# Performance work log

Measured on AMD Instinct MI355X. Metric: run time of the kernel, lower is better.

Reference implementation:

```python
import jax, jax.numpy as jnp
import numpy as np

N_NODES = 40000


def setup_inputs() -> dict:
    key = jax.random.key(0)
    k_h, k_w, k_b, k_s, k_d = jax.random.split(key, 5)
    in_feats, out_feats, n_edges = 128, 128, 640000
    h = jax.random.normal(k_h, (N_NODES, in_feats), dtype=jnp.float32)
    # nn.Linear(in_feats, out_feats): weight [out, in], bias [out]
    W = jax.random.normal(k_w, (out_feats, in_feats), dtype=jnp.float32) * (1.0 / np.sqrt(in_feats))
    b = jax.random.normal(k_b, (out_feats,), dtype=jnp.float32) * 0.01
    src = jax.random.randint(k_s, (n_edges,), 0, N_NODES, dtype=jnp.int32)
    dst = jax.random.randint(k_d, (n_edges,), 0, N_NODES, dtype=jnp.int32)
    return {"h": h, "W": W, "b": b, "src": src, "dst": dst}


def reference(h, W, b, src, dst):
    # update_all(copy_u('h','m'), sum('m','h_N')):
    # gather messages from source nodes, segment-sum into destination nodes.
    msgs = h[src]                                              # [E, in_feats] irregular gather
    agg = jax.ops.segment_sum(msgs, dst, num_segments=N_NODES)  # [N, in_feats] scatter-add
    # Source module applies the linear to h (agg is computed but unused there);
    # we return agg as a second output so the SpMM is observable.
    out = h @ W.T + b                                          # [N, out_feats]
    return out, agg
```

## Files before the change

kernel.cpp:

```cpp
#include <hip/hip_runtime.h>

#define FEAT 128
#define CAP  64

typedef short bf16x8 __attribute__((ext_vector_type(8)));
typedef float f32x4  __attribute__((ext_vector_type(4)));

__device__ __forceinline__ unsigned pack_bf16x2(float x, float y) {
    unsigned ux = __float_as_uint(x);
    ux = (ux + 0x7fffu + ((ux >> 16) & 1u)) >> 16;
    unsigned uy = __float_as_uint(y);
    uy = (uy + 0x7fffu + ((uy >> 16) & 1u)) & 0xffff0000u;
    return uy | ux;
}

__device__ __forceinline__ bf16x8 pack8(float4 a, float4 b) {
    uint4 u = make_uint4(pack_bf16x2(a.x, a.y), pack_bf16x2(a.z, a.w),
                         pack_bf16x2(b.x, b.y), pack_bf16x2(b.z, b.w));
    return __builtin_bit_cast(bf16x8, u);
}

__device__ __forceinline__ f32x4 unpack2(unsigned x, unsigned y) {
    return (f32x4){__uint_as_float(x << 16), __uint_as_float(x & 0xffff0000u),
                   __uint_as_float(y << 16), __uint_as_float(y & 0xffff0000u)};
}

__global__ __launch_bounds__(256) void fused_kernel(
    const float* __restrict__ h, const float* __restrict__ W,
    const float* __restrict__ b, const int* __restrict__ src,
    const int* __restrict__ dst, float* __restrict__ out,
    uint4* __restrict__ hb4, int* __restrict__ counts, int* __restrict__ bucket,
    int nrows, int gemm_blocks, int E)
{
    const int bid = blockIdx.x;
    const int tid = threadIdx.x;

    if (bid >= gemm_blocks) {
        int e = (bid - gemm_blocks) * 256 + tid;
        if (e < E) {
            int d = dst[e];
            int pos = atomicAdd(&counts[d], 1);
            if (pos < CAP) bucket[d * CAP + pos] = src[e];
        }
        return;
    }

    const int wid  = bid * 4 + (tid >> 6);
    const int lane = tid & 63;
    const int m    = lane & 15, quad = lane >> 4;
    const int r0g  = wid * 32;
    if (r0g >= nrows) return;

    const float4* __restrict__ h4 = (const float4*)h;
    const float4* __restrict__ W4 = (const float4*)W;

    bf16x8 af[2][4];
#pragma unroll
    for (int mt = 0; mt < 2; ++mt) {
        int gr = r0g + mt * 16 + m;
#pragma unroll
        for (int ks = 0; ks < 4; ++ks) {
            float4 a0 = h4[(size_t)gr * 32 + ks * 8 + quad * 2];
            float4 a1 = h4[(size_t)gr * 32 + ks * 8 + quad * 2 + 1];
            af[mt][ks] = pack8(a0, a1);
        }
    }

#pragma unroll
    for (int mt = 0; mt < 2; ++mt) {
        int gr = r0g + mt * 16 + m;
        if (gr < nrows) {
#pragma unroll
            for (int ks = 0; ks < 4; ++ks)
                hb4[(size_t)gr * 16 + ks * 4 + quad] = __builtin_bit_cast(uint4, af[mt][ks]);
        }
    }

    f32x4 acc[2][8];
#pragma unroll
    for (int mt = 0; mt < 2; ++mt)
#pragma unroll
        for (int n = 0; n < 8; ++n) acc[mt][n] = (f32x4){0.f, 0.f, 0.f, 0.f};

#pragma unroll
    for (int n = 0; n < 8; ++n) {
        int c = n * 16 + m;
#pragma unroll
        for (int ks = 0; ks < 4; ++ks) {
            float4 b0 = W4[(size_t)c * 32 + ks * 8 + quad * 2];
            float4 b1 = W4[(size_t)c * 32 + ks * 8 + quad * 2 + 1];
            bf16x8 bf = pack8(b0, b1);
#pragma unroll
            for (int mt = 0; mt < 2; ++mt)
                acc[mt][n] = __builtin_amdgcn_mfma_f32_16x16x32_bf16(
                    af[mt][ks], bf, acc[mt][n], 0, 0, 0);
        }
    }

#pragma unroll
    for (int n = 0; n < 8; ++n) {
        float bias = b[n * 16 + m];
#pragma unroll
        for (int mt = 0; mt < 2; ++mt)
#pragma unroll
            for (int r = 0; r < 4; ++r) {
                int gr = r0g + mt * 16 + quad * 4 + r;
                if (gr < nrows) out[(size_t)gr * FEAT + n * 16 + m] = acc[mt][n][r] + bias;
            }
    }
}

__global__ __launch_bounds__(256) void gather_bucket_kernel(
    const uint4* __restrict__ hb4, const int* __restrict__ counts,
    const int* __restrict__ bucket, float* __restrict__ agg, int N)
{
    int gid  = blockIdx.x * 256 + threadIdx.x;
    int node = gid >> 6;
    int lane = gid & 63;
    if (node >= N) return;

    int deg = counts[node];
    deg = (deg > CAP) ? CAP : deg;
    int eid = (lane < deg) ? bucket[node * CAP + lane] : 0;

    const int q = lane >> 4, ql = lane & 15;

    f32x4 al0 = {0.f,0.f,0.f,0.f}, ah0 = {0.f,0.f,0.f,0.f};
    f32x4 al1 = {0.f,0.f,0.f,0.f}, ah1 = {0.f,0.f,0.f,0.f};

    int t = 0;
    for (; t + 8 <= deg; t += 8) {
        int s0 = __shfl(eid, t + q);
        int s1 = __shfl(eid, t + 4 + q);
        uint4 v0 = hb4[(size_t)s0 * 16 + ql];
        uint4 v1 = hb4[(size_t)s1 * 16 + ql];
        al0 += unpack2(v0.x, v0.y);
        ah0 += unpack2(v0.z, v0.w);
        al1 += unpack2(v1.x, v1.y);
        ah1 += unpack2(v1.z, v1.w);
    }
    {
        int i0 = t + q, i1 = t + 4 + q;
        int s0 = __shfl(eid, i0 & 63);
        int s1 = __shfl(eid, i1 & 63);
        if (i0 < deg) {
            uint4 v = hb4[(size_t)s0 * 16 + ql];
            al0 += unpack2(v.x, v.y);
            ah0 += unpack2(v.z, v.w);
        }
        if (i1 < deg) {
            uint4 v = hb4[(size_t)s1 * 16 + ql];
            al1 += unpack2(v.x, v.y);
            ah1 += unpack2(v.z, v.w);
        }
    }
    al0 += al1; ah0 += ah1;

#pragma unroll
    for (int j = 0; j < 4; ++j) {
        al0[j] += __shfl_down(al0[j], 32);
        ah0[j] += __shfl_down(ah0[j], 32);
        al0[j] += __shfl_down(al0[j], 16);
        ah0[j] += __shfl_down(ah0[j], 16);
    }

    if (q == 0) {
        ((float4*)agg)[(size_t)node * 32 + ql * 2]     = make_float4(al0[0], al0[1], al0[2], al0[3]);
        ((float4*)agg)[(size_t)node * 32 + ql * 2 + 1] = make_float4(ah0[0], ah0[1], ah0[2], ah0[3]);
    }
}

__global__ __launch_bounds__(256, 2) void gemm_f32_kernel(
    const float* __restrict__ h, const float* __restrict__ W,
    const float* __restrict__ b, float* __restrict__ out, int nrows)
{
    __shared__ float4 wsh[128 * 8];
    __shared__ float4 hsh[64 * 8];
    const int tid = threadIdx.x;
    const int tx  = tid & 31;
    const int ty  = tid >> 5;
    const int r0  = blockIdx.x * 64;
    const float4* __restrict__ W4 = (const float4*)W;
    const float4* __restrict__ h4 = (const float4*)h;
    float acc[8][4];
#pragma unroll
    for (int i = 0; i < 8; ++i)
#pragma unroll
        for (int j = 0; j < 4; ++j) acc[i][j] = 0.f;
    for (int p = 0; p < 4; ++p) {
        if (p) __syncthreads();
#pragma unroll
        for (int l = 0; l < 4; ++l) {
            int flat = l * 256 + tid;
            int c = flat >> 3, kc = flat & 7;
            wsh[c * 8 + (kc ^ ((c >> 2) & 7))] = W4[c * 32 + p * 8 + kc];
        }
#pragma unroll
        for (int l = 0; l < 2; ++l) {
            int flat = l * 256 + tid;
            int r = flat >> 3, kc = flat & 7;
            int gr = r0 + r;
            float4 v = make_float4(0.f, 0.f, 0.f, 0.f);
            if (gr < nrows) v = h4[(size_t)gr * 32 + p * 8 + kc];
            hsh[r * 8 + (kc ^ ((r >> 2) & 7))] = v;
        }
        __syncthreads();
#pragma unroll
        for (int kc = 0; kc < 8; ++kc) {
            float4 wv[4], hv[8];
#pragma unroll
            for (int j = 0; j < 4; ++j) wv[j] = wsh[(4 * tx + j) * 8 + (kc ^ (tx & 7))];
#pragma unroll
            for (int i = 0; i < 8; ++i) {
                int r = 8 * ty + i;
                hv[i] = hsh[r * 8 + (kc ^ ((r >> 2) & 7))];
            }
#pragma unroll
            for (int i = 0; i < 8; ++i)
#pragma unroll
                for (int j = 0; j < 4; ++j) {
                    acc[i][j] += hv[i].x * wv[j].x;
                    acc[i][j] += hv[i].y * wv[j].y;
                    acc[i][j] += hv[i].z * wv[j].z;
                    acc[i][j] += hv[i].w * wv[j].w;
                }
        }
    }
    const float4 bj = ((const float4*)b)[tx];
    float4* out4 = (float4*)out;
#pragma unroll
    for (int i = 0; i < 8; ++i) {
        int gr = r0 + 8 * ty + i;
        if (gr < nrows) {
            float4 o;
            o.x = acc[i][0] + bj.x; o.y = acc[i][1] + bj.y;
            o.z = acc[i][2] + bj.z; o.w = acc[i][3] + bj.w;
            out4[(size_t)gr * 32 + tx] = o;
        }
    }
}

__global__ __launch_bounds__(256) void scatter_add_kernel(
    const float* __restrict__ h, const int* __restrict__ src,
    const int* __restrict__ dst, float* __restrict__ agg, int E)
{
    int gid  = blockIdx.x * 256 + threadIdx.x;
    int e    = gid >> 6;
    int lane = gid & 63;
    if (e >= E) return;
    int s = src[e];
    int d = dst[e];
    const float2* hp = (const float2*)(h + (size_t)s * FEAT);
    float2 v = hp[lane];
    float* ap = agg + (size_t)d * FEAT + 2 * lane;
    unsafeAtomicAdd(ap,     v.x);
    unsafeAtomicAdd(ap + 1, v.y);
}

extern "C" void kernel_launch(void* const* d_in, const int* in_sizes, int n_in,
                              void* d_out, int out_size, void* d_ws, size_t ws_size,
                              hipStream_t stream) {
    const float* h   = (const float*)d_in[0];
    const float* W   = (const float*)d_in[1];
    const float* b   = (const float*)d_in[2];
    const int*   src = (const int*)d_in[3];
    const int*   dst = (const int*)d_in[4];

    const int n = in_sizes[0] / FEAT;
    const int E = in_sizes[3];

    float* out = (float*)d_out;
    float* agg = out + (size_t)n * FEAT;

    size_t hb_bytes     = (size_t)n * FEAT * 2;
    size_t bucket_bytes = (size_t)n * CAP * 4;
    size_t counts_bytes = (size_t)n * 4;
    size_t need = hb_bytes + bucket_bytes + counts_bytes;

    if (ws_size >= need) {
        uint4* hb     = (uint4*)d_ws;
        int*   bucket = (int*)((char*)d_ws + hb_bytes);
        int*   counts = (int*)((char*)d_ws + hb_bytes + bucket_bytes);

        hipMemsetAsync(counts, 0, counts_bytes, stream);

        int gemm_blocks = (n + 127) / 128;
        int fill_blocks = (E + 255) / 256;
        fused_kernel<<<dim3(gemm_blocks + fill_blocks), dim3(256), 0, stream>>>(
            h, W, b, src, dst, out, hb, counts, bucket, n, gemm_blocks, E);

        gather_bucket_kernel<<<dim3((int)(((long long)n * 64 + 255) / 256)), dim3(256), 0, stream>>>(
            hb, counts, bucket, agg, n);
    } else {
        gemm_f32_kernel<<<dim3((n + 63) / 64), dim3(256), 0, stream>>>(h, W, b, out, n);
        hipMemsetAsync(agg, 0, (size_t)n * FEAT * sizeof(float), stream);
        int nblocks = (int)(((long long)E * 64 + 255) / 256);
        scatter_add_kernel<<<dim3(nblocks), dim3(256), 0, stream>>>(h, src, dst, agg, E);
    }
}
```

Measured before the change: 147.5 us.

## Batch bucket-fill atomics, pad counters, split GEMM columns, use nontemporal stores

The bucket-fill path now handles four edges per thread, issuing all loads, then all atomics, then all stores, so more memory operations are in flight. Per-node counters are padded to a 16-int stride to spread atomic contention across cache lines. The GEMM part now splits each 32-row tile's output columns across two waves, which doubles the GEMM blocks and halves accumulator registers, at the cost of loading h twice. Output and agg writes become nontemporal stores to avoid polluting cache. The padded counters need a larger workspace and a bigger memset.

```diff
diff --git a/kernel.cpp b/kernel.cpp
--- a/kernel.cpp
+++ b/kernel.cpp
@@ -2,6 +2,7 @@
 
 #define FEAT 128
 #define CAP  64
+#define CSTRIDE 16
 
 typedef short bf16x8 __attribute__((ext_vector_type(8)));
 typedef float f32x4  __attribute__((ext_vector_type(4)));
@@ -36,19 +37,31 @@
     const int tid = threadIdx.x;
 
     if (bid >= gemm_blocks) {
-        int e = (bid - gemm_blocks) * 256 + tid;
-        if (e < E) {
-            int d = dst[e];
-            int pos = atomicAdd(&counts[d], 1);
-            if (pos < CAP) bucket[d * CAP + pos] = src[e];
+        int base = (bid - gemm_blocks) * 1024 + tid;
+        int dk[4], sk[4], pk[4];
+#pragma unroll
+        for (int k = 0; k < 4; ++k) {
+            int e = base + k * 256;
+            if (e < E) { dk[k] = dst[e]; sk[k] = src[e]; }
+        }
+#pragma unroll
+        for (int k = 0; k < 4; ++k) {
+            int e = base + k * 256;
+            if (e < E) pk[k] = atomicAdd(&counts[dk[k] * CSTRIDE], 1);
+        }
+#pragma unroll
+        for (int k = 0; k < 4; ++k) {
+            int e = base + k * 256;
+            if (e < E && pk[k] < CAP) bucket[dk[k] * CAP + pk[k]] = sk[k];
         }
         return;
     }
 
-    const int wid  = bid * 4 + (tid >> 6);
+    const int w    = tid >> 6;
     const int lane = tid & 63;
     const int m    = lane & 15, quad = lane >> 4;
-    const int r0g  = wid * 32;
+    const int r0g  = bid * 64 + (w >> 1) * 32;
+    const int ch   = w & 1;
     if (r0g >= nrows) return;
 
     const float4* __restrict__ h4 = (const float4*)h;
@@ -66,25 +79,27 @@
         }
     }
 
-#pragma unroll
-    for (int mt = 0; mt < 2; ++mt) {
-        int gr = r0g + mt * 16 + m;
-        if (gr < nrows) {
-#pragma unroll
-            for (int ks = 0; ks < 4; ++ks)
-                hb4[(size_t)gr * 16 + ks * 4 + quad] = __builtin_bit_cast(uint4, af[mt][ks]);
-        }
-    }
-
-    f32x4 acc[2][8];
+    if (ch == 0) {
+#pragma unroll
+        for (int mt = 0; mt < 2; ++mt) {
+            int gr = r0g + mt * 16 + m;
+            if (gr < nrows) {
+#pragma unroll
+                for (int ks = 0; ks < 4; ++ks)
+                    hb4[(size_t)gr * 16 + ks * 4 + quad] = __builtin_bit_cast(uint4, af[mt][ks]);
+            }
+        }
+    }
+
+    f32x4 acc[2][4];
 #pragma unroll
     for (int mt = 0; mt < 2; ++mt)
 #pragma unroll
-        for (int n = 0; n < 8; ++n) acc[mt][n] = (f32x4){0.f, 0.f, 0.f, 0.f};
-
-#pragma unroll
-    for (int n = 0; n < 8; ++n) {
-        int c = n * 16 + m;
+        for (int n = 0; n < 4; ++n) acc[mt][n] = (f32x4){0.f, 0.f, 0.f, 0.f};
+
+#pragma unroll
+    for (int n = 0; n < 4; ++n) {
+        int c = (ch * 4 + n) * 16 + m;
 #pragma unroll
         for (int ks = 0; ks < 4; ++ks) {
             float4 b0 = W4[(size_t)c * 32 + ks * 8 + quad * 2];
@@ -98,14 +113,17 @@
     }
 
 #pragma unroll
-    for (int n = 0; n < 8; ++n) {
-        float bias = b[n * 16 + m];
+    for (int n = 0; n < 4; ++n) {
+        int col = (ch * 4 + n) * 16 + m;
+        float bias = b[col];
 #pragma unroll
         for (int mt = 0; mt < 2; ++mt)
 #pragma unroll
             for (int r = 0; r < 4; ++r) {
                 int gr = r0g + mt * 16 + quad * 4 + r;
-                if (gr < nrows) out[(size_t)gr * FEAT + n * 16 + m] = acc[mt][n][r] + bias;
+                if (gr < nrows)
+                    __builtin_nontemporal_store(acc[mt][n][r] + bias,
+                                                &out[(size_t)gr * FEAT + col]);
             }
     }
 }
@@ -119,7 +137,7 @@
     int lane = gid & 63;
     if (node >= N) return;
 
-    int deg = counts[node];
+    int deg = counts[node * CSTRIDE];
     deg = (deg > CAP) ? CAP : deg;
     int eid = (lane < deg) ? bucket[node * CAP + lane] : 0;
 
@@ -165,8 +183,9 @@
     }
 
     if (q == 0) {
-        ((float4*)agg)[(size_t)node * 32 + ql * 2]     = make_float4(al0[0], al0[1], al0[2], al0[3]);
-        ((float4*)agg)[(size_t)node * 32 + ql * 2 + 1] = make_float4(ah0[0], ah0[1], ah0[2], ah0[3]);
+        f32x4* aggv = (f32x4*)agg;
+        __builtin_nontemporal_store(al0, &aggv[(size_t)node * 32 + ql * 2]);
+        __builtin_nontemporal_store(ah0, &aggv[(size_t)node * 32 + ql * 2 + 1]);
     }
 }
 
@@ -274,7 +293,7 @@
 
     size_t hb_bytes     = (size_t)n * FEAT * 2;
     size_t bucket_bytes = (size_t)n * CAP * 4;
-    size_t counts_bytes = (size_t)n * 4;
+    size_t counts_bytes = (size_t)n * CSTRIDE * 4;
     size_t need = hb_bytes + bucket_bytes + counts_bytes;
 
     if (ws_size >= need) {
@@ -282,10 +301,10 @@
         int*   bucket = (int*)((char*)d_ws + hb_bytes);
         int*   counts = (int*)((char*)d_ws + hb_bytes + bucket_bytes);
 
-        hipMemsetAsync(counts, 0, counts_bytes, stream);
-
-        int gemm_blocks = (n + 127) / 128;
-        int fill_blocks = (E + 255) / 256;
+        (void)hipMemsetAsync(counts, 0, counts_bytes, stream);
+
+        int gemm_blocks = (n + 63) / 64;
+        int fill_blocks = (E + 1023) / 1024;
         fused_kernel<<<dim3(gemm_blocks + fill_blocks), dim3(256), 0, stream>>>(
             h, W, b, src, dst, out, hb, counts, bucket, n, gemm_blocks, E);
 
@@ -293,7 +312,7 @@
             hb, counts, bucket, agg, n);
     } else {
         gemm_f32_kernel<<<dim3((n + 63) / 64), dim3(256), 0, stream>>>(h, W, b, out, n);
-        hipMemsetAsync(agg, 0, (size_t)n * FEAT * sizeof(float), stream);
+        (void)hipMemsetAsync(agg, 0, (size_t)n * FEAT * sizeof(float), stream);
         int nblocks = (int)(((long long)E * 64 + 255) / 256);
         scatter_add_kernel<<<dim3(nblocks), dim3(256), 0, stream>>>(h, src, dst, agg, E);
     }
```

Measured after the change: 144.7 us. No clear change (-1.9%).
